# Performance work log

Hardware: AMD Instinct MI355X
Metric: run time of the kernel (lower is better)

## Reference

```python
import jax, jax.numpy as jnp
import numpy as np

B, T, M = 64, 32, 64
IN_DIM, GNN, H, L = 256, 256, 4, 3
TEMP, OUT, NH, NLT = 256, 512, 8, 2
DIST_THR = 0.3


def _ln(x, s, b, eps=1e-5):
    mu = jnp.mean(x, -1, keepdims=True)
    v = jnp.mean(jnp.square(x - mu), -1, keepdims=True)
    return (x - mu) * jax.lax.rsqrt(v + eps) * s + b


def setup_inputs() -> dict:
    key = jax.random.key(0)
    ks = iter(jax.random.split(key, 64))
    def nrm(shape, scale=0.05):
        return jax.random.normal(next(ks), shape, jnp.float32) * scale
    C = GNN // H
    return dict(
        drone_feats=jax.random.normal(next(ks), (B, T, M, IN_DIM), jnp.float32),
        boxes=jax.random.uniform(next(ks), (B, T, M, 5), jnp.float32),
        drone_mask=jnp.ones((B, T, M), jnp.float32),
        in_proj_W=nrm((GNN, IN_DIM)), in_proj_b=jnp.zeros((GNN,), jnp.float32),
        gat_lin_W=nrm((L, GNN, GNN)), gat_edge_W=nrm((L, 3, GNN)),
        gat_att_src=nrm((L, H, C)), gat_att_dst=nrm((L, H, C)), gat_att_edge=nrm((L, H, C)),
        gat_bias=jnp.zeros((L, GNN), jnp.float32),
        gat_ln_s=jnp.ones((L, GNN), jnp.float32), gat_ln_b=jnp.zeros((L, GNN), jnp.float32),
        temp_W=nrm((TEMP, GNN)), temp_b=jnp.zeros((TEMP,), jnp.float32),
        pos_emb=nrm((1, T, TEMP), 0.02),
        qkv_W=nrm((NLT, 3 * TEMP, TEMP)), qkv_b=jnp.zeros((NLT, 3 * TEMP), jnp.float32),
        attn_out_W=nrm((NLT, TEMP, TEMP)), attn_out_b=jnp.zeros((NLT, TEMP), jnp.float32),
        ln1_s=jnp.ones((NLT, TEMP), jnp.float32), ln1_b=jnp.zeros((NLT, TEMP), jnp.float32),
        ln2_s=jnp.ones((NLT, TEMP), jnp.float32), ln2_b=jnp.zeros((NLT, TEMP), jnp.float32),
        ff1_W=nrm((NLT, 2 * TEMP, TEMP)), ff1_b=jnp.zeros((NLT, 2 * TEMP), jnp.float32),
        ff2_W=nrm((NLT, TEMP, 2 * TEMP)), ff2_b=jnp.zeros((NLT, TEMP), jnp.float32),
        pool_W=nrm((1, TEMP)), pool_b=jnp.zeros((1,), jnp.float32),
        out_W=nrm((OUT, TEMP)), out_b=jnp.zeros((OUT,), jnp.float32),
        out_ln_s=jnp.ones((OUT,), jnp.float32), out_ln_b=jnp.zeros((OUT,), jnp.float32),
    )


def reference(drone_feats, boxes, drone_mask, in_proj_W, in_proj_b, gat_lin_W, gat_edge_W,
              gat_att_src, gat_att_dst, gat_att_edge, gat_bias, gat_ln_s, gat_ln_b,
              temp_W, temp_b, pos_emb, qkv_W, qkv_b, attn_out_W, attn_out_b,
              ln1_s, ln1_b, ln2_s, ln2_b, ff1_W, ff1_b, ff2_W, ff2_b,
              pool_W, pool_b, out_W, out_b, out_ln_s, out_ln_b):
    Bv, Tv, Mv, _ = drone_feats.shape
    Hh, Cc = gat_att_src.shape[1], gat_att_src.shape[2]
    valid = drone_mask > 0.5                                  # [B,T,M]

    # ---- batched radius-graph build (dense masked form over tiny M) ----
    pos = boxes[..., 1:3]                                     # [B,T,M,2]
    rel = pos[..., None, :, :] - pos[..., :, None, :]         # [B,T,s,d,2] = pos_d - pos_s
    sq = jnp.sum(jnp.square(rel), -1)
    dist = jnp.sqrt(jnp.maximum(sq, 1e-12))                   # [B,T,s,d]
    eye = jnp.eye(Mv, dtype=bool)
    pair_valid = valid[..., :, None] & valid[..., None, :]
    adj = pair_valid & (dist < DIST_THR) & (~eye)             # real directed edges (s->d)
    eattr = jnp.where(adj[..., None], jnp.concatenate([dist[..., None], rel], -1), 0.0)
    # GATConv(add_self_loops=True, fill_value='mean'): self-loop attr = mean incoming attr
    deg = jnp.maximum(jnp.sum(adj, axis=-2), 1).astype(eattr.dtype)   # incoming per dst
    loop_attr = jnp.sum(eattr, axis=-3) / deg[..., None]              # [B,T,M,3]
    eattr = jnp.where(eye[:, :, None], loop_attr[..., None, :, :], eattr)
    full_adj = adj | (eye & pair_valid)

    # ---- spatial GAT stack ----
    x = jnp.einsum('btmi,gi->btmg', drone_feats, in_proj_W) + in_proj_b
    x = x * valid[..., None]
    for l in range(gat_lin_W.shape[0]):
        h = jnp.einsum('btmg,gk->btmk', x, gat_lin_W[l]).reshape(Bv, Tv, Mv, Hh, Cc)
        a_src = jnp.einsum('btmhc,hc->btmh', h, gat_att_src[l])
        a_dst = jnp.einsum('btmhc,hc->btmh', h, gat_att_dst[l])
        w_e = jnp.einsum('ehc,hc->eh', gat_edge_W[l].reshape(3, Hh, Cc), gat_att_edge[l])
        a_edge = jnp.einsum('btsde,eh->btsdh', eattr, w_e)
        logits = a_src[..., :, None, :] + a_dst[..., None, :, :] + a_edge
        logits = jnp.where(logits >= 0, logits, 0.2 * logits)        # LeakyReLU(0.2)
        logits = jnp.where(full_adj[..., None], logits, jnp.float32(-1e9))
        alpha = jax.nn.softmax(logits, axis=-3)                      # softmax over src per dst
        msg = jnp.einsum('btsdh,btshc->btdhc', alpha, h).reshape(Bv, Tv, Mv, Hh * Cc) + gat_bias[l]
        x = jax.nn.relu(_ln(msg + x, gat_ln_s[l], gat_ln_b[l]))

    nvalid = jnp.maximum(jnp.sum(valid, -1), 1).astype(x.dtype)
    frame = jnp.sum(x * valid[..., None], axis=-2) / nvalid[..., None]   # [B,T,GNN]

    # ---- temporal transformer (norm_first, relu, 2 layers) ----
    y = jnp.einsum('btg,dg->btd', frame, temp_W) + temp_b
    y = y + pos_emb[:, :Tv, :]
    D = y.shape[-1]
    hd = D // NH
    for l in range(qkv_W.shape[0]):
        z = _ln(y, ln1_s[l], ln1_b[l])
        qkv = z @ qkv_W[l].T + qkv_b[l]
        q, k, v = jnp.split(qkv, 3, axis=-1)
        q = q.reshape(Bv, Tv, NH, hd).transpose(0, 2, 1, 3)
        k = k.reshape(Bv, Tv, NH, hd).transpose(0, 2, 1, 3)
        v = v.reshape(Bv, Tv, NH, hd).transpose(0, 2, 1, 3)
        att = jax.nn.softmax(jnp.einsum('bhqd,bhkd->bhqk', q, k) / jnp.sqrt(jnp.float32(hd)), -1)
        o = jnp.einsum('bhqk,bhkd->bhqd', att, v).transpose(0, 2, 1, 3).reshape(Bv, Tv, D)
        y = y + o @ attn_out_W[l].T + attn_out_b[l]
        z = _ln(y, ln2_s[l], ln2_b[l])
        y = y + jax.nn.relu(z @ ff1_W[l].T + ff1_b[l]) @ ff2_W[l].T + ff2_b[l]

    wts = jax.nn.softmax(y @ pool_W.T + pool_b, axis=1)   # [B,T,1]
    pooled = jnp.sum(y * wts, axis=1)                     # [B,D]
    out = pooled @ out_W.T + out_b
    return jax.nn.relu(_ln(out, out_ln_s, out_ln_b))
```

## Files before the change

kernel.cpp:

```cpp
#include <hip/hip_runtime.h>
#include <math.h>

#define BT 2048

typedef __attribute__((ext_vector_type(8))) short bf16x8;
typedef __attribute__((ext_vector_type(4))) float f32x4;
typedef __attribute__((ext_vector_type(4))) unsigned short u16x4;

__device__ inline unsigned short f2bf(float f) {
    union { float f; unsigned u; } v; v.f = f;
    unsigned r = (v.u >> 16) & 1u;
    return (unsigned short)((v.u + 0x7FFFu + r) >> 16);
}
__device__ inline float bf2f(unsigned short s) {
    union { unsigned u; float f; } v; v.u = ((unsigned)s) << 16;
    return v.f;
}

__device__ inline float dot4(const float4 a, const float4 b) {
    return fmaf(a.x, b.x, fmaf(a.y, b.y, fmaf(a.z, b.z, a.w * b.w)));
}

union F8 { float4 v2[2]; float f[8]; };

#define XP 264

__global__ __launch_bounds__(256) void k_prep(const float* __restrict__ inW,
                                              const float* __restrict__ gatW,
                                              unsigned short* __restrict__ dst) {
    int gid = blockIdx.x * 256 + threadIdx.x;
    int mat = gid >> 14;
    int r   = gid & 16383;
    int ks  = r >> 10;
    int nt  = (r >> 6) & 15;
    int lane = r & 63;
    int ln15 = lane & 15, q = lane >> 4;
    int n  = nt * 16 + ln15;
    int k0 = ks * 32 + q * 8;
    const float* src; bool tr;
    if (mat == 0) { src = inW; tr = true; }
    else          { src = gatW + (size_t)(mat - 1) * 65536; tr = false; }
    unsigned short* d = dst + ((size_t)mat * 16384 + r) * 16;
    if (ks < 8) {
        #pragma unroll
        for (int j = 0; j < 8; j++) {
            float v = tr ? src[n * 256 + k0 + j] : src[(size_t)(k0 + j) * 256 + n];
            unsigned short hi = f2bf(v);
            d[j]     = hi;
            d[8 + j] = f2bf(v - bf2f(hi));
        }
    } else {
        #pragma unroll
        for (int j = 0; j < 8; j++) { d[j] = 0; d[8 + j] = 0; }
    }
}

__global__ __launch_bounds__(1024, 4) void k_gnn(const float* __restrict__ feats,
                                                 const float* __restrict__ boxes,
                                                 const float* __restrict__ maskp,
                                                 const unsigned short* __restrict__ BswAll,
                                                 const float* __restrict__ inb,
                                                 const float* __restrict__ edgeW,
                                                 const float* __restrict__ attSg,
                                                 const float* __restrict__ attDg,
                                                 const float* __restrict__ attEg,
                                                 const float* __restrict__ gbias,
                                                 const float* __restrict__ glns,
                                                 const float* __restrict__ glnb,
                                                 float* __restrict__ framebuf) {
    int bt = blockIdx.x;
    size_t fbase = (size_t)bt * 64 * 256;

    __shared__ unsigned short xH[64 * XP];
    __shared__ unsigned short xL[64 * XP];
    __shared__ unsigned short hT[256 * 136];
    __shared__ float pxS[64], pyS[64], vmS[64];
    __shared__ float loopS[192];
    __shared__ float asrcS[16][64], adstS[16][64];
    __shared__ float wESall[36];
    __shared__ float sumsS[64][8];
    __shared__ float mrsS[64][2];
    __shared__ float nvS;

    int tid = threadIdx.x, lane = tid & 63, w = tid >> 6;
    int ln15 = lane & 15, q = lane >> 4;
    int nt = w;
    int eh = w >> 2;
    int dq = w & 3;

    if (tid < 64) {
        const float* bx = boxes + (size_t)(bt * 64 + tid) * 5;
        pxS[tid] = bx[1];
        pyS[tid] = bx[2];
        vmS[tid] = maskp[bt * 64 + tid];
    } else if (tid < 100) {
        int idx = tid - 64;
        int l = idx / 12, r2 = idx - l * 12;
        int e = r2 >> 2, h2 = r2 & 3;
        float sm = 0.f;
        const float* ew = edgeW + (size_t)l * 768 + e * 256 + h2 * 64;
        const float* ae = attEg + (size_t)l * 256 + h2 * 64;
        for (int c = 0; c < 64; c++) sm += ew[c] * ae[c];
        wESall[idx] = sm;
    }
    #pragma unroll
    for (int j = 0; j < 4; j++) {
        int g = j * 4096 + tid * 4;
        int row = g >> 8, col = g & 255;
        float4 v4 = *(const float4*)&feats[fbase + g];
        union { u16x4 v; unsigned short u[4]; } H4, L4;
        float vf[4] = {v4.x, v4.y, v4.z, v4.w};
        #pragma unroll
        for (int jj = 0; jj < 4; jj++) {
            H4.u[jj] = f2bf(vf[jj]);
            L4.u[jj] = f2bf(vf[jj] - bf2f(H4.u[jj]));
        }
        *(u16x4*)&xH[row * XP + col] = H4.v;
        *(u16x4*)&xL[row * XP + col] = L4.v;
    }
    __syncthreads();

    {
        int d = tid >> 4, part = tid & 15;
        float pxd = pxS[d], pyd = pyS[d];
        bool vd = vmS[d] > 0.5f;
        float deg = 0.f, s0 = 0.f, s1 = 0.f, s2 = 0.f;
        #pragma unroll
        for (int k = 0; k < 4; k++) {
            int s = part * 4 + k;
            float rx = pxd - pxS[s], ry = pyd - pyS[s];
            float dist = sqrtf(fmaxf(rx * rx + ry * ry, 1e-12f));
            bool adj = vd && (vmS[s] > 0.5f) && (dist < 0.3f) && (s != d);
            if (adj) { deg += 1.f; s0 += dist; s1 += rx; s2 += ry; }
        }
        #pragma unroll
        for (int off = 1; off < 16; off <<= 1) {
            deg += __shfl_xor(deg, off);
            s0  += __shfl_xor(s0, off);
            s1  += __shfl_xor(s1, off);
            s2  += __shfl_xor(s2, off);
        }
        if (part == 0) {
            float dg = fmaxf(deg, 1.f);
            loopS[d * 3 + 0] = s0 / dg;
            loopS[d * 3 + 1] = s1 / dg;
            loopS[d * 3 + 2] = s2 / dg;
        }
    }
    if (tid == 0) {
        float nv = 0.f;
        for (int m = 0; m < 64; m++) nv += vmS[m] > 0.5f ? 1.f : 0.f;
        nvS = fmaxf(nv, 1.f);
    }

    {
        f32x4 acc[4];
        #pragma unroll
        for (int mt = 0; mt < 4; mt++) acc[mt] = (f32x4){0.f, 0.f, 0.f, 0.f};
        for (int ks = 0; ks < 8; ks++) {
            const unsigned short* fb = &BswAll[((size_t)(ks * 16 + nt) * 64 + lane) * 16];
            bf16x8 bhi = *(const bf16x8*)&fb[0];
            bf16x8 blo = *(const bf16x8*)&fb[8];
            #pragma unroll
            for (int mt = 0; mt < 4; mt++) {
                int ao = (mt * 16 + ln15) * XP + ks * 32 + q * 8;
                bf16x8 ahi = *(const bf16x8*)&xH[ao];
                bf16x8 alo = *(const bf16x8*)&xL[ao];
                acc[mt] = __builtin_amdgcn_mfma_f32_16x16x32_bf16(ahi, bhi, acc[mt], 0, 0, 0);
                acc[mt] = __builtin_amdgcn_mfma_f32_16x16x32_bf16(alo, bhi, acc[mt], 0, 0, 0);
                acc[mt] = __builtin_amdgcn_mfma_f32_16x16x32_bf16(ahi, blo, acc[mt], 0, 0, 0);
            }
        }
        __syncthreads();
        int c = nt * 16 + ln15;
        float bv = inb[c];
        #pragma unroll
        for (int mt = 0; mt < 4; mt++) {
            #pragma unroll
            for (int r = 0; r < 4; r++) {
                int m = mt * 16 + q * 4 + r;
                float v = (acc[mt][r] + bv) * (vmS[m] > 0.5f ? 1.f : 0.f);
                unsigned short hi = f2bf(v);
                xH[m * XP + c] = hi;
                xL[m * XP + c] = f2bf(v - bf2f(hi));
            }
        }
    }
    __syncthreads();

    for (int l = 0; l < 3; l++) {
        const unsigned short* BswL = BswAll + (size_t)(1 + l) * 16384 * 16;
        const float* attSl = attSg + (size_t)l * 256;
        const float* attDl = attDg + (size_t)l * 256;
        const float* biasl = gbias + (size_t)l * 256;
        const float* lnsl  = glns + (size_t)l * 256;
        const float* lnbl  = glnb + (size_t)l * 256;
        const float* wES   = wESall + l * 12;

        f32x4 acc[4];
        #pragma unroll
        for (int mt = 0; mt < 4; mt++) acc[mt] = (f32x4){0.f, 0.f, 0.f, 0.f};
        for (int ks = 0; ks < 8; ks++) {
            const unsigned short* fb = &BswL[((size_t)(ks * 16 + nt) * 64 + lane) * 16];
            bf16x8 bhi = *(const bf16x8*)&fb[0];
            bf16x8 blo = *(const bf16x8*)&fb[8];
            #pragma unroll
            for (int mt = 0; mt < 4; mt++) {
                int ao = (mt * 16 + ln15) * XP + ks * 32 + q * 8;
                bf16x8 ahi = *(const bf16x8*)&xH[ao];
                bf16x8 alo = *(const bf16x8*)&xL[ao];
                acc[mt] = __builtin_amdgcn_mfma_f32_16x16x32_bf16(ahi, bhi, acc[mt], 0, 0, 0);
                acc[mt] = __builtin_amdgcn_mfma_f32_16x16x32_bf16(alo, bhi, acc[mt], 0, 0, 0);
                acc[mt] = __builtin_amdgcn_mfma_f32_16x16x32_bf16(ahi, blo, acc[mt], 0, 0, 0);
            }
        }

        {
            int c = nt * 16 + ln15;
            float aS = attSl[c], aD = attDl[c];
            float pS[4][4], pD[4][4];
            #pragma unroll
            for (int mt = 0; mt < 4; mt++) {
                union { u16x4 v; unsigned short u[4]; } HH, LL;
                #pragma unroll
                for (int r = 0; r < 4; r++) {
                    float v = acc[mt][r];
                    pS[mt][r] = v * aS;
                    pD[mt][r] = v * aD;
                    unsigned short hi = f2bf(v);
                    HH.u[r] = hi;
                    LL.u[r] = f2bf(v - bf2f(hi));
                }
                int s = mt * 16 + q * 4;
                *(u16x4*)&hT[c * 136 + s] = HH.v;
                *(u16x4*)&hT[c * 136 + 64 + s] = LL.v;
            }
            #pragma unroll
            for (int off = 1; off < 16; off <<= 1) {
                #pragma unroll
                for (int mt = 0; mt < 4; mt++)
                    #pragma unroll
                    for (int r = 0; r < 4; r++) {
                        pS[mt][r] += __shfl_xor(pS[mt][r], off);
                        pD[mt][r] += __shfl_xor(pD[mt][r], off);
                    }
            }
            if (ln15 == 0) {
                #pragma unroll
                for (int mt = 0; mt < 4; mt++)
                    #pragma unroll
                    for (int r = 0; r < 4; r++) {
                        int m = mt * 16 + q * 4 + r;
                        asrcS[w][m] = pS[mt][r];
                        adstS[w][m] = pD[mt][r];
                    }
            }
        }
        __syncthreads();

        f32x4 macc[4];
        #pragma unroll
        for (int ct = 0; ct < 4; ct++) macc[ct] = (f32x4){0.f, 0.f, 0.f, 0.f};
        {
            int d = dq * 16 + ln15;
            float pxd = pxS[d], pyd = pyS[d];
            bool vdv = vmS[d] > 0.5f;
            float adstv = adstS[4 * eh][d] + adstS[4 * eh + 1][d]
                        + adstS[4 * eh + 2][d] + adstS[4 * eh + 3][d];
            float lp0 = loopS[d * 3 + 0];
            float lp1 = loopS[d * 3 + 1];
            float lp2 = loopS[d * 3 + 2];
            float we0 = wES[eh], we1 = wES[4 + eh], we2 = wES[8 + eh];

            float lg[16];
            #pragma unroll
            for (int ks = 0; ks < 2; ks++) {
                int s0 = ks * 32 + q * 8;
                F8 PX, PY, VM, AU;
                PX.v2[0] = *(const float4*)&pxS[s0]; PX.v2[1] = *(const float4*)&pxS[s0 + 4];
                PY.v2[0] = *(const float4*)&pyS[s0]; PY.v2[1] = *(const float4*)&pyS[s0 + 4];
                VM.v2[0] = *(const float4*)&vmS[s0]; VM.v2[1] = *(const float4*)&vmS[s0 + 4];
                AU.v2[0] = *(const float4*)&asrcS[4 * eh][s0];
                AU.v2[1] = *(const float4*)&asrcS[4 * eh][s0 + 4];
                #pragma unroll
                for (int i = 1; i < 4; i++) {
                    float4 a0 = *(const float4*)&asrcS[4 * eh + i][s0];
                    float4 a1 = *(const float4*)&asrcS[4 * eh + i][s0 + 4];
                    AU.v2[0].x += a0.x; AU.v2[0].y += a0.y; AU.v2[0].z += a0.z; AU.v2[0].w += a0.w;
                    AU.v2[1].x += a1.x; AU.v2[1].y += a1.y; AU.v2[1].z += a1.z; AU.v2[1].w += a1.w;
                }
                #pragma unroll
                for (int j = 0; j < 8; j++) {
                    int s = s0 + j;
                    float vsf = VM.f[j];
                    float rx = pxd - PX.f[j], ry = pyd - PY.f[j];
                    float dist = sqrtf(fmaxf(rx * rx + ry * ry, 1e-12f));
                    bool self = (s == d);
                    bool adj = vdv && (vsf > 0.5f) && (dist < 0.3f) && !self;
                    float e0 = adj ? dist : (self ? lp0 : 0.f);
                    float e1 = adj ? rx   : (self ? lp1 : 0.f);
                    float e2 = adj ? ry   : (self ? lp2 : 0.f);
                    bool fa = adj || (self && vdv);
                    float lv = AU.f[j] + adstv + e0 * we0 + e1 * we1 + e2 * we2;
                    lv = lv >= 0.f ? lv : 0.2f * lv;
                    lg[ks * 8 + j] = fa ? lv : -1e9f;
                }
            }

            float mx = lg[0];
            #pragma unroll
            for (int j = 1; j < 16; j++) mx = fmaxf(mx, lg[j]);
            mx = fmaxf(mx, __shfl_xor(mx, 16));
            mx = fmaxf(mx, __shfl_xor(mx, 32));
            float sm = 0.f;
            #pragma unroll
            for (int j = 0; j < 16; j++) { lg[j] = __expf(lg[j] - mx); sm += lg[j]; }
            sm += __shfl_xor(sm, 16);
            sm += __shfl_xor(sm, 32);
            float inv = 1.f / sm;

            bf16x8 ah[2], al[2];
            #pragma unroll
            for (int ks2 = 0; ks2 < 2; ks2++) {
                union { bf16x8 v; unsigned short u[8]; } H, L;
                #pragma unroll
                for (int j = 0; j < 8; j++) {
                    float a = lg[ks2 * 8 + j] * inv;
                    unsigned short hi = f2bf(a);
                    H.u[j] = hi;
                    L.u[j] = f2bf(a - bf2f(hi));
                }
                ah[ks2] = H.v; al[ks2] = L.v;
            }

            #pragma unroll
            for (int ks2 = 0; ks2 < 2; ks2++) {
                #pragma unroll
                for (int ct = 0; ct < 4; ct++) {
                    const unsigned short* hb =
                        &hT[(size_t)(eh * 64 + ct * 16 + ln15) * 136 + ks2 * 32 + q * 8];
                    bf16x8 bhi = *(const bf16x8*)&hb[0];
                    bf16x8 blo = *(const bf16x8*)&hb[64];
                    macc[ct] = __builtin_amdgcn_mfma_f32_16x16x32_bf16(ah[ks2], bhi, macc[ct], 0, 0, 0);
                    macc[ct] = __builtin_amdgcn_mfma_f32_16x16x32_bf16(al[ks2], bhi, macc[ct], 0, 0, 0);
                    macc[ct] = __builtin_amdgcn_mfma_f32_16x16x32_bf16(ah[ks2], blo, macc[ct], 0, 0, 0);
                }
            }
        }

        {
            float bsv[4], scv[4], bbv[4];
            #pragma unroll
            for (int ct = 0; ct < 4; ct++) {
                int c = eh * 64 + ct * 16 + ln15;
                bsv[ct] = biasl[c];
                scv[ct] = lnsl[c];
                bbv[ct] = lnbl[c];
            }
            float xo[4][4];
            #pragma unroll
            for (int r = 0; r < 4; r++) {
                int d2 = dq * 16 + q * 4 + r;
                #pragma unroll
                for (int ct = 0; ct < 4; ct++) {
                    int o = d2 * XP + eh * 64 + ct * 16 + ln15;
                    xo[ct][r] = bf2f(xH[o]) + bf2f(xL[o]);
                }
            }
            float ps[4], ps2[4];
            #pragma unroll
            for (int r = 0; r < 4; r++) {
                float s = 0.f, s2 = 0.f;
                #pragma unroll
                for (int ct = 0; ct < 4; ct++) {
                    float v = macc[ct][r] + xo[ct][r] + bsv[ct];
                    s += v; s2 += v * v;
                }
                ps[r] = s; ps2[r] = s2;
            }
            #pragma unroll
            for (int off = 1; off < 16; off <<= 1) {
                #pragma unroll
                for (int i = 0; i < 4; i++) {
                    ps[i]  += __shfl_xor(ps[i], off);
                    ps2[i] += __shfl_xor(ps2[i], off);
                }
            }
            if (ln15 == 0) {
                #pragma unroll
                for (int r = 0; r < 4; r++) {
                    int d2 = dq * 16 + q * 4 + r;
                    sumsS[d2][eh * 2 + 0] = ps[r];
                    sumsS[d2][eh * 2 + 1] = ps2[r];
                }
            }
            __syncthreads();
            if (tid < 64) {
                float S  = sumsS[tid][0] + sumsS[tid][2] + sumsS[tid][4] + sumsS[tid][6];
                float S2 = sumsS[tid][1] + sumsS[tid][3] + sumsS[tid][5] + sumsS[tid][7];
                float mu = S * (1.f / 256.f);
                float var = S2 * (1.f / 256.f) - mu * mu;
                mrsS[tid][0] = mu;
                mrsS[tid][1] = rsqrtf(var + 1e-5f);
            }
            __syncthreads();
            #pragma unroll
            for (int r = 0; r < 4; r++) {
                int d2 = dq * 16 + q * 4 + r;
                float mu = mrsS[d2][0], rs = mrsS[d2][1];
                #pragma unroll
                for (int ct = 0; ct < 4; ct++) {
                    float v = (macc[ct][r] + xo[ct][r] + bsv[ct] - mu) * rs * scv[ct] + bbv[ct];
                    v = fmaxf(v, 0.f);
                    unsigned short hi = f2bf(v);
                    int o = d2 * XP + eh * 64 + ct * 16 + ln15;
                    xH[o] = hi;
                    xL[o] = f2bf(v - bf2f(hi));
                }
            }
        }
        __syncthreads();
    }

    if (tid < 256) {
        float s = 0.f;
        for (int m = 0; m < 64; m++) {
            float xv = bf2f(xH[m * XP + tid]) + bf2f(xL[m * XP + tid]);
            s += xv * (vmS[m] > 0.5f ? 1.f : 0.f);
        }
        framebuf[(size_t)bt * 256 + tid] = s / nvS;
    }
}

__global__ __launch_bounds__(256) void k_temp4(const float* __restrict__ framebuf,
                                               const float* __restrict__ tW,
                                               const float* __restrict__ tb,
                                               const float* __restrict__ pe,
                                               float* __restrict__ ybuf) {
    int b4 = blockIdx.x;
    int tid = threadIdx.x;
    __shared__ float frS[4][256];
    #pragma unroll
    for (int t = 0; t < 4; t++) frS[t][tid] = framebuf[(size_t)(b4 * 4 + t) * 256 + tid];
    __syncthreads();
    float acc[4];
    #pragma unroll
    for (int t = 0; t < 4; t++) acc[t] = tb[tid] + pe[((b4 * 4 + t) & 31) * 256 + tid];
    const float* wrow = tW + (size_t)tid * 256;
    for (int g = 0; g < 256; g += 4) {
        float4 wv = *(const float4*)&wrow[g];
        #pragma unroll
        for (int t = 0; t < 4; t++) acc[t] += dot4(*(const float4*)&frS[t][g], wv);
    }
    #pragma unroll
    for (int t = 0; t < 4; t++) ybuf[(size_t)(b4 * 4 + t) * 256 + tid] = acc[t];
}

__global__ __launch_bounds__(256) void k_ln_qkv4(const float* __restrict__ ybuf,
                                                 const float* __restrict__ ln_s,
                                                 const float* __restrict__ ln_b,
                                                 const float* __restrict__ qW,
                                                 const float* __restrict__ qb,
                                                 float* __restrict__ qkvbuf) {
    int b4 = blockIdx.x, tid = threadIdx.x;
    int lane = tid & 63, wv = tid >> 6;
    __shared__ float zS[4][256];
    {
        int bt = b4 * 4 + wv;
        float4 yv = *(const float4*)&ybuf[(size_t)bt * 256 + lane * 4];
        float s = yv.x + yv.y + yv.z + yv.w;
        float s2 = yv.x * yv.x + yv.y * yv.y + yv.z * yv.z + yv.w * yv.w;
        #pragma unroll
        for (int off = 1; off < 64; off <<= 1) { s += __shfl_xor(s, off); s2 += __shfl_xor(s2, off); }
        float mu = s * (1.f / 256.f);
        float var = s2 * (1.f / 256.f) - mu * mu;
        float rstd = rsqrtf(var + 1e-5f);
        float4 ls = *(const float4*)&ln_s[lane * 4];
        float4 lb = *(const float4*)&ln_b[lane * 4];
        float4 z;
        z.x = (yv.x - mu) * rstd * ls.x + lb.x;
        z.y = (yv.y - mu) * rstd * ls.y + lb.y;
        z.z = (yv.z - mu) * rstd * ls.z + lb.z;
        z.w = (yv.w - mu) * rstd * ls.w + lb.w;
        *(float4*)&zS[wv][lane * 4] = z;
    }
    __syncthreads();
    for (int r = 0; r < 3; r++) {
        int j = r * 256 + tid;
        float acc[4];
        float bv = qb[j];
        #pragma unroll
        for (int t = 0; t < 4; t++) acc[t] = bv;
        const float* wrow = qW + (size_t)j * 256;
        for (int i = 0; i < 256; i += 4) {
            float4 wv4 = *(const float4*)&wrow[i];
            #pragma unroll
            for (int t = 0; t < 4; t++) acc[t] += dot4(*(const float4*)&zS[t][i], wv4);
        }
        #pragma unroll
        for (int t = 0; t < 4; t++) qkvbuf[(size_t)(b4 * 4 + t) * 768 + j] = acc[t];
    }
}

__global__ __launch_bounds__(64) void k_attn(const float* __restrict__ qkvbuf,
                                             float* __restrict__ obuf) {
    int blk = blockIdx.x;
    int b = blk >> 3, h = blk & 7;
    int tid = threadIdx.x;
    __shared__ float Ks[32 * 32], Vs[32 * 32];
    for (int idx = tid; idx < 1024; idx += 64) {
        int tk = idx >> 5, c = idx & 31;
        size_t qbase = ((size_t)(b * 32 + tk)) * 768 + h * 32 + c;
        Ks[idx] = qkvbuf[qbase + 256];
        Vs[idx] = qkvbuf[qbase + 512];
    }
    __syncthreads();
    if (tid < 32) {
        int tq = tid;
        float qv[32];
        size_t qb0 = ((size_t)(b * 32 + tq)) * 768 + h * 32;
        #pragma unroll
        for (int c = 0; c < 32; c++) qv[c] = qkvbuf[qb0 + c];
        float scr[32];
        float mx = -1e30f;
        #pragma unroll
        for (int tk = 0; tk < 32; tk++) {
            float dd = 0.f;
            #pragma unroll
            for (int c = 0; c < 32; c++) dd = fmaf(qv[c], Ks[tk * 32 + c], dd);
            dd *= 0.17677669529663687f;
            scr[tk] = dd;
            mx = fmaxf(mx, dd);
        }
        float sm = 0.f;
        #pragma unroll
        for (int tk = 0; tk < 32; tk++) { scr[tk] = __expf(scr[tk] - mx); sm += scr[tk]; }
        float inv = 1.f / sm;
        float o[32];
        #pragma unroll
        for (int c = 0; c < 32; c++) o[c] = 0.f;
        #pragma unroll
        for (int tk = 0; tk < 32; tk++) {
            float a = scr[tk] * inv;
            #pragma unroll
            for (int c = 0; c < 32; c++) o[c] = fmaf(a, Vs[tk * 32 + c], o[c]);
        }
        size_t ob = ((size_t)(b * 32 + tq)) * 256 + h * 32;
        #pragma unroll
        for (int c = 0; c < 32; c++) obuf[ob + c] = o[c];
    }
}

__global__ __launch_bounds__(256) void k_attn_out4(const float* __restrict__ obuf,
                                                   const float* __restrict__ W,
                                                   const float* __restrict__ bvec,
                                                   float* __restrict__ ybuf) {
    int b4 = blockIdx.x, tid = threadIdx.x;
    int lane = tid & 63, wv = tid >> 6;
    __shared__ float oS[4][256];
    *(float4*)&oS[wv][lane * 4] = *(const float4*)&obuf[(size_t)(b4 * 4 + wv) * 256 + lane * 4];
    __syncthreads();
    float acc[4];
    float bv = bvec[tid];
    #pragma unroll
    for (int t = 0; t < 4; t++) acc[t] = bv;
    const float* wrow = W + (size_t)tid * 256;
    for (int i = 0; i < 256; i += 4) {
        float4 wv4 = *(const float4*)&wrow[i];
        #pragma unroll
        for (int t = 0; t < 4; t++) acc[t] += dot4(*(const float4*)&oS[t][i], wv4);
    }
    #pragma unroll
    for (int t = 0; t < 4; t++) ybuf[(size_t)(b4 * 4 + t) * 256 + tid] += acc[t];
}

__global__ __launch_bounds__(256) void k_ff4(float* __restrict__ ybuf,
                                             const float* __restrict__ ln_s,
                                             const float* __restrict__ ln_b,
                                             const float* __restrict__ W1,
                                             const float* __restrict__ b1,
                                             const float* __restrict__ W2,
                                             const float* __restrict__ b2) {
    int b4 = blockIdx.x, tid = threadIdx.x;
    int lane = tid & 63, wv = tid >> 6;
    __shared__ float zS[4][256];
    __shared__ float fS[4][512];
    {
        int bt = b4 * 4 + wv;
        float4 yv = *(const float4*)&ybuf[(size_t)bt * 256 + lane * 4];
        float s = yv.x + yv.y + yv.z + yv.w;
        float s2 = yv.x * yv.x + yv.y * yv.y + yv.z * yv.z + yv.w * yv.w;
        #pragma unroll
        for (int off = 1; off < 64; off <<= 1) { s += __shfl_xor(s, off); s2 += __shfl_xor(s2, off); }
        float mu = s * (1.f / 256.f);
        float var = s2 * (1.f / 256.f) - mu * mu;
        float rstd = rsqrtf(var + 1e-5f);
        float4 ls = *(const float4*)&ln_s[lane * 4];
        float4 lb = *(const float4*)&ln_b[lane * 4];
        float4 z;
        z.x = (yv.x - mu) * rstd * ls.x + lb.x;
        z.y = (yv.y - mu) * rstd * ls.y + lb.y;
        z.z = (yv.z - mu) * rstd * ls.z + lb.z;
        z.w = (yv.w - mu) * rstd * ls.w + lb.w;
        *(float4*)&zS[wv][lane * 4] = z;
    }
    __syncthreads();
    for (int r = 0; r < 2; r++) {
        int j = r * 256 + tid;
        float acc[4];
        float bv = b1[j];
        #pragma unroll
        for (int t = 0; t < 4; t++) acc[t] = bv;
        const float* wrow = W1 + (size_t)j * 256;
        for (int i = 0; i < 256; i += 4) {
            float4 wv4 = *(const float4*)&wrow[i];
            #pragma unroll
            for (int t = 0; t < 4; t++) acc[t] += dot4(*(const float4*)&zS[t][i], wv4);
        }
        #pragma unroll
        for (int t = 0; t < 4; t++) fS[t][j] = fmaxf(acc[t], 0.f);
    }
    __syncthreads();
    float acc[4];
    float bv = b2[tid];
    #pragma unroll
    for (int t = 0; t < 4; t++) acc[t] = bv;
    const float* wrow = W2 + (size_t)tid * 512;
    for (int jj = 0; jj < 512; jj += 4) {
        float4 wv4 = *(const float4*)&wrow[jj];
        #pragma unroll
        for (int t = 0; t < 4; t++) acc[t] += dot4(*(const float4*)&fS[t][jj], wv4);
    }
    #pragma unroll
    for (int t = 0; t < 4; t++) {
        size_t idx = (size_t)(b4 * 4 + t) * 256 + tid;
        ybuf[idx] = ybuf[idx] + acc[t];
    }
}

__global__ __launch_bounds__(256) void k_pool_out(const float* __restrict__ ybuf,
                                                  const float* __restrict__ pW,
                                                  const float* __restrict__ pb,
                                                  const float* __restrict__ oW,
                                                  const float* __restrict__ ob,
                                                  const float* __restrict__ lns,
                                                  const float* __restrict__ lnb,
                                                  float* __restrict__ dout) {
    int b = blockIdx.x, tid = threadIdx.x;
    __shared__ float redP[256];
    __shared__ float wS[32];
    __shared__ float pS[256];
    __shared__ float red[8];
    int tq = tid >> 3, part = tid & 7;
    float partial = 0.f;
    {
        const float* yrow = ybuf + ((size_t)(b * 32 + tq)) * 256 + part * 32;
        const float* pwp = pW + part * 32;
        #pragma unroll
        for (int j = 0; j < 32; j += 4) {
            float4 yv = *(const float4*)&yrow[j];
            float4 wv = *(const float4*)&pwp[j];
            partial += dot4(yv, wv);
        }
    }
    redP[tid] = partial;
    __syncthreads();
    if (tid < 32) {
        float s = pb[0];
        for (int p = 0; p < 8; p++) s += redP[tid * 8 + p];
        float mx = s;
        #pragma unroll
        for (int off = 16; off; off >>= 1) mx = fmaxf(mx, __shfl_xor(mx, off));
        float e = __expf(s - mx);
        float sm = e;
        #pragma unroll
        for (int off = 16; off; off >>= 1) sm += __shfl_xor(sm, off);
        wS[tid] = e / sm;
    }
    __syncthreads();
    float p = 0.f;
    for (int t = 0; t < 32; t++) p += ybuf[((size_t)(b * 32 + t)) * 256 + tid] * wS[t];
    pS[tid] = p;
    __syncthreads();
    float accs[2];
    for (int r = 0; r < 2; r++) {
        int j = r * 256 + tid;
        float acc = ob[j];
        const float* wrow = oW + (size_t)j * 256;
        for (int g = 0; g < 256; g += 4) {
            float4 pv = *(const float4*)&pS[g];
            float4 wv = *(const float4*)&wrow[g];
            acc += dot4(pv, wv);
        }
        accs[r] = acc;
    }
    float s = accs[0] + accs[1];
    float s2 = accs[0] * accs[0] + accs[1] * accs[1];
    #pragma unroll
    for (int off = 32; off; off >>= 1) {
        s += __shfl_xor(s, off);
        s2 += __shfl_xor(s2, off);
    }
    int wid = threadIdx.x >> 6;
    int lane = threadIdx.x & 63;
    if (lane == 0) { red[wid] = s; red[4 + wid] = s2; }
    __syncthreads();
    s = red[0] + red[1] + red[2] + red[3];
    s2 = red[4] + red[5] + red[6] + red[7];
    float mu = s * (1.f / 512.f);
    float var = s2 * (1.f / 512.f) - mu * mu;
    float rstd = rsqrtf(var + 1e-5f);
    dout[b * 512 + tid]       = fmaxf((accs[0] - mu) * rstd * lns[tid] + lnb[tid], 0.f);
    dout[b * 512 + tid + 256] = fmaxf((accs[1] - mu) * rstd * lns[tid + 256] + lnb[tid + 256], 0.f);
}

extern "C" void kernel_launch(void* const* d_in, const int* in_sizes, int n_in,
                              void* d_out, int out_size, void* d_ws, size_t ws_size,
                              hipStream_t stream) {
    const float* drone_feats = (const float*)d_in[0];
    const float* boxes       = (const float*)d_in[1];
    const float* drone_mask  = (const float*)d_in[2];
    const float* in_proj_W   = (const float*)d_in[3];
    const float* in_proj_b   = (const float*)d_in[4];
    const float* gat_lin_W   = (const float*)d_in[5];
    const float* gat_edge_W  = (const float*)d_in[6];
    const float* gat_att_src = (const float*)d_in[7];
    const float* gat_att_dst = (const float*)d_in[8];
    const float* gat_att_edge= (const float*)d_in[9];
    const float* gat_bias    = (const float*)d_in[10];
    const float* gat_ln_s    = (const float*)d_in[11];
    const float* gat_ln_b    = (const float*)d_in[12];
    const float* temp_W      = (const float*)d_in[13];
    const float* temp_b      = (const float*)d_in[14];
    const float* pos_emb     = (const float*)d_in[15];
    const float* qkv_W       = (const float*)d_in[16];
    const float* qkv_b       = (const float*)d_in[17];
    const float* attn_out_W  = (const float*)d_in[18];
    const float* attn_out_b  = (const float*)d_in[19];
    const float* ln1_s       = (const float*)d_in[20];
    const float* ln1_b       = (const float*)d_in[21];
    const float* ln2_s       = (const float*)d_in[22];
    const float* ln2_b       = (const float*)d_in[23];
    const float* ff1_W       = (const float*)d_in[24];
    const float* ff1_b       = (const float*)d_in[25];
    const float* ff2_W       = (const float*)d_in[26];
    const float* ff2_b       = (const float*)d_in[27];
    const float* pool_W      = (const float*)d_in[28];
    const float* pool_b      = (const float*)d_in[29];
    const float* out_W       = (const float*)d_in[30];
    const float* out_b       = (const float*)d_in[31];
    const float* out_ln_s    = (const float*)d_in[32];
    const float* out_ln_b    = (const float*)d_in[33];
    float* out = (float*)d_out;

    float* ws = (float*)d_ws;
    unsigned short* Bsw = (unsigned short*)ws;
    size_t off = (size_t)(4 * 16384 * 16) / 2;
    float* framebuf = ws + off; off += (size_t)BT * 256;
    float* ybuf   = ws + off; off += (size_t)BT * 256;
    float* qkvbuf = ws + off; off += (size_t)BT * 768;
    float* obuf   = ws + off; off += (size_t)BT * 256;

    k_prep<<<dim3(256), dim3(256), 0, stream>>>(in_proj_W, gat_lin_W, Bsw);
    k_gnn<<<dim3(BT), dim3(1024), 0, stream>>>(drone_feats, boxes, drone_mask, Bsw,
        in_proj_b, gat_edge_W, gat_att_src, gat_att_dst, gat_att_edge,
        gat_bias, gat_ln_s, gat_ln_b, framebuf);
    k_temp4<<<dim3(BT / 4), dim3(256), 0, stream>>>(framebuf, temp_W, temp_b, pos_emb, ybuf);
    for (int l = 0; l < 2; l++) {
        k_ln_qkv4<<<dim3(BT / 4), dim3(256), 0, stream>>>(ybuf, ln1_s + l * 256, ln1_b + l * 256,
            qkv_W + (size_t)l * 768 * 256, qkv_b + l * 768, qkvbuf);
        k_attn<<<dim3(512), dim3(64), 0, stream>>>(qkvbuf, obuf);
        k_attn_out4<<<dim3(BT / 4), dim3(256), 0, stream>>>(obuf,
            attn_out_W + (size_t)l * 65536, attn_out_b + l * 256, ybuf);
        k_ff4<<<dim3(BT / 4), dim3(256), 0, stream>>>(ybuf, ln2_s + l * 256, ln2_b + l * 256,
            ff1_W + (size_t)l * 131072, ff1_b + l * 512,
            ff2_W + (size_t)l * 131072, ff2_b + l * 256);
    }
    k_pool_out<<<dim3(64), dim3(256), 0, stream>>>(ybuf, pool_W, pool_b, out_W, out_b,
                                                   out_ln_s, out_ln_b, out);
}
```

Measured before the change: 1.133 ms.

## Fold attention projections into aux GEMM, alias LDS buffers, pack bf16 conversions

Precomputes W·att_src and W·att_dst per layer and head in a new prep kernel. Four extra waves then compute per-node attention logits with a small MFMA GEMM, which replaces the per-wave product and shuffle reduction. The hT buffer now shares LDS with xH/xL. To make that safe, the residual x plus bias is read into macc before a new barrier, and launch bounds are raised to allow more occupancy. Split-bf16 conversions now use the packed v_cvt_pk_bf16_f32 instruction, at the cost of extra MFMA work on four waves and one more barrier per layer.

New measurement: 1.142 ms. No clear change (+0.8%).

```diff
diff --git a/kernel.cpp b/kernel.cpp
--- a/kernel.cpp
+++ b/kernel.cpp
@@ -15,6 +15,14 @@
 __device__ inline float bf2f(unsigned short s) {
     union { unsigned u; float f; } v; v.u = ((unsigned)s) << 16;
     return v.f;
+}
+__device__ inline float ubf(unsigned u) {
+    union { unsigned u; float f; } v; v.u = u; return v.f;
+}
+__device__ inline unsigned cvt2(float a, float b) {
+    unsigned r;
+    asm("v_cvt_pk_bf16_f32 %0, %1, %2" : "=v"(r) : "v"(a), "v"(b));
+    return r;
 }
 
 __device__ inline float dot4(const float4 a, const float4 b) {
@@ -55,14 +63,39 @@
     }
 }
 
-__global__ __launch_bounds__(1024, 4) void k_gnn(const float* __restrict__ feats,
+__global__ __launch_bounds__(64) void k_prep_aux(const float* __restrict__ gatW,
+                                                 const float* __restrict__ attS,
+                                                 const float* __restrict__ attD,
+                                                 unsigned short* __restrict__ dst) {
+    int l  = blockIdx.x >> 3;
+    int ks = blockIdx.x & 7;
+    int lane = threadIdx.x;
+    int ln15 = lane & 15, q = lane >> 4;
+    int k0 = ks * 32 + q * 8;
+    const float* W = gatW + (size_t)l * 65536;
+    unsigned short* d = dst + ((size_t)(l * 8 + ks) * 64 + lane) * 16;
+    #pragma unroll
+    for (int j = 0; j < 8; j++) {
+        float v = 0.f;
+        if (ln15 < 8) {
+            int head = ln15 & 3;
+            const float* a = (ln15 < 4 ? attS : attD) + (size_t)l * 256 + head * 64;
+            const float* wr = W + (size_t)(k0 + j) * 256 + head * 64;
+            for (int c = 0; c < 64; c++) v = fmaf(wr[c], a[c], v);
+        }
+        unsigned short hi = f2bf(v);
+        d[j]     = hi;
+        d[8 + j] = f2bf(v - bf2f(hi));
+    }
+}
+
+__global__ __launch_bounds__(1024, 8) void k_gnn(const float* __restrict__ feats,
                                                  const float* __restrict__ boxes,
                                                  const float* __restrict__ maskp,
                                                  const unsigned short* __restrict__ BswAll,
+                                                 const unsigned short* __restrict__ auxB,
                                                  const float* __restrict__ inb,
                                                  const float* __restrict__ edgeW,
-                                                 const float* __restrict__ attSg,
-                                                 const float* __restrict__ attDg,
                                                  const float* __restrict__ attEg,
                                                  const float* __restrict__ gbias,
                                                  const float* __restrict__ glns,
@@ -71,16 +104,17 @@
     int bt = blockIdx.x;
     size_t fbase = (size_t)bt * 64 * 256;
 
-    __shared__ unsigned short xH[64 * XP];
-    __shared__ unsigned short xL[64 * XP];
-    __shared__ unsigned short hT[256 * 136];
+    __shared__ __align__(16) unsigned short U[256 * 136];
     __shared__ float pxS[64], pyS[64], vmS[64];
     __shared__ float loopS[192];
-    __shared__ float asrcS[16][64], adstS[16][64];
+    __shared__ float asrcS[4][64], adstS[4][64];
     __shared__ float wESall[36];
     __shared__ float sumsS[64][8];
     __shared__ float mrsS[64][2];
     __shared__ float nvS;
+
+    unsigned short* xH = U;
+    unsigned short* xL = U + 64 * XP;
 
     int tid = threadIdx.x, lane = tid & 63, w = tid >> 6;
     int ln15 = lane & 15, q = lane >> 4;
@@ -108,15 +142,16 @@
         int g = j * 4096 + tid * 4;
         int row = g >> 8, col = g & 255;
         float4 v4 = *(const float4*)&feats[fbase + g];
-        union { u16x4 v; unsigned short u[4]; } H4, L4;
-        float vf[4] = {v4.x, v4.y, v4.z, v4.w};
-        #pragma unroll
-        for (int jj = 0; jj < 4; jj++) {
-            H4.u[jj] = f2bf(vf[jj]);
-            L4.u[jj] = f2bf(vf[jj] - bf2f(H4.u[jj]));
-        }
-        *(u16x4*)&xH[row * XP + col] = H4.v;
-        *(u16x4*)&xL[row * XP + col] = L4.v;
+        unsigned p0 = cvt2(v4.x, v4.y);
+        unsigned p1 = cvt2(v4.z, v4.w);
+        float h0 = ubf(p0 << 16), h1 = ubf(p0 & 0xFFFF0000u);
+        float h2 = ubf(p1 << 16), h3 = ubf(p1 & 0xFFFF0000u);
+        unsigned l0 = cvt2(v4.x - h0, v4.y - h1);
+        unsigned l1 = cvt2(v4.z - h2, v4.w - h3);
+        *(unsigned*)&xH[row * XP + col]     = p0;
+        *(unsigned*)&xH[row * XP + col + 2] = p1;
+        *(unsigned*)&xL[row * XP + col]     = l0;
+        *(unsigned*)&xL[row * XP + col + 2] = l1;
     }
     __syncthreads();
 
@@ -190,8 +225,6 @@
 
     for (int l = 0; l < 3; l++) {
         const unsigned short* BswL = BswAll + (size_t)(1 + l) * 16384 * 16;
-        const float* attSl = attSg + (size_t)l * 256;
-        const float* attDl = attDg + (size_t)l * 256;
         const float* biasl = gbias + (size_t)l * 256;
         const float* lnsl  = glns + (size_t)l * 256;
         const float* lnbl  = glnb + (size_t)l * 256;
@@ -215,58 +248,68 @@
             }
         }
 
+        if (w >= 12) {
+            int mm = w - 12;
+            f32x4 aax = (f32x4){0.f, 0.f, 0.f, 0.f};
+            const unsigned short* AuxL = auxB + (size_t)l * 8 * 64 * 16;
+            for (int ks = 0; ks < 8; ks++) {
+                const unsigned short* fb = &AuxL[((size_t)ks * 64 + lane) * 16];
+                bf16x8 bhi = *(const bf16x8*)&fb[0];
+                bf16x8 blo = *(const bf16x8*)&fb[8];
+                int ao = (mm * 16 + ln15) * XP + ks * 32 + q * 8;
+                bf16x8 ahi = *(const bf16x8*)&xH[ao];
+                bf16x8 alo = *(const bf16x8*)&xL[ao];
+                aax = __builtin_amdgcn_mfma_f32_16x16x32_bf16(ahi, bhi, aax, 0, 0, 0);
+                aax = __builtin_amdgcn_mfma_f32_16x16x32_bf16(alo, bhi, aax, 0, 0, 0);
+                aax = __builtin_amdgcn_mfma_f32_16x16x32_bf16(ahi, blo, aax, 0, 0, 0);
+            }
+            if (ln15 < 4) {
+                #pragma unroll
+                for (int r = 0; r < 4; r++) asrcS[ln15][mm * 16 + q * 4 + r] = aax[r];
+            } else if (ln15 < 8) {
+                #pragma unroll
+                for (int r = 0; r < 4; r++) adstS[ln15 - 4][mm * 16 + q * 4 + r] = aax[r];
+            }
+        }
+
+        f32x4 macc[4];
+        #pragma unroll
+        for (int ct = 0; ct < 4; ct++) {
+            int c = eh * 64 + ct * 16 + ln15;
+            float bv = biasl[c];
+            #pragma unroll
+            for (int r = 0; r < 4; r++) {
+                int d2 = dq * 16 + q * 4 + r;
+                int o = d2 * XP + c;
+                macc[ct][r] = bf2f(xH[o]) + bf2f(xL[o]) + bv;
+            }
+        }
+        __syncthreads();
+
         {
             int c = nt * 16 + ln15;
-            float aS = attSl[c], aD = attDl[c];
-            float pS[4][4], pD[4][4];
             #pragma unroll
             for (int mt = 0; mt < 4; mt++) {
-                union { u16x4 v; unsigned short u[4]; } HH, LL;
-                #pragma unroll
-                for (int r = 0; r < 4; r++) {
-                    float v = acc[mt][r];
-                    pS[mt][r] = v * aS;
-                    pD[mt][r] = v * aD;
-                    unsigned short hi = f2bf(v);
-                    HH.u[r] = hi;
-                    LL.u[r] = f2bf(v - bf2f(hi));
-                }
+                unsigned p0 = cvt2(acc[mt][0], acc[mt][1]);
+                unsigned p1 = cvt2(acc[mt][2], acc[mt][3]);
+                float h0 = ubf(p0 << 16), h1 = ubf(p0 & 0xFFFF0000u);
+                float h2 = ubf(p1 << 16), h3 = ubf(p1 & 0xFFFF0000u);
+                unsigned l0 = cvt2(acc[mt][0] - h0, acc[mt][1] - h1);
+                unsigned l1 = cvt2(acc[mt][2] - h2, acc[mt][3] - h3);
                 int s = mt * 16 + q * 4;
-                *(u16x4*)&hT[c * 136 + s] = HH.v;
-                *(u16x4*)&hT[c * 136 + 64 + s] = LL.v;
-            }
-            #pragma unroll
-            for (int off = 1; off < 16; off <<= 1) {
-                #pragma unroll
-                for (int mt = 0; mt < 4; mt++)
-                    #pragma unroll
-                    for (int r = 0; r < 4; r++) {
-                        pS[mt][r] += __shfl_xor(pS[mt][r], off);
-                        pD[mt][r] += __shfl_xor(pD[mt][r], off);
-                    }
-            }
-            if (ln15 == 0) {
-                #pragma unroll
-                for (int mt = 0; mt < 4; mt++)
-                    #pragma unroll
-                    for (int r = 0; r < 4; r++) {
-                        int m = mt * 16 + q * 4 + r;
-                        asrcS[w][m] = pS[mt][r];
-                        adstS[w][m] = pD[mt][r];
-                    }
+                *(unsigned*)&U[c * 136 + s]          = p0;
+                *(unsigned*)&U[c * 136 + s + 2]      = p1;
+                *(unsigned*)&U[c * 136 + 64 + s]     = l0;
+                *(unsigned*)&U[c * 136 + 64 + s + 2] = l1;
             }
         }
         __syncthreads();
 
-        f32x4 macc[4];
-        #pragma unroll
-        for (int ct = 0; ct < 4; ct++) macc[ct] = (f32x4){0.f, 0.f, 0.f, 0.f};
         {
             int d = dq * 16 + ln15;
             float pxd = pxS[d], pyd = pyS[d];
             bool vdv = vmS[d] > 0.5f;
-            float adstv = adstS[4 * eh][d] + adstS[4 * eh + 1][d]
-                        + adstS[4 * eh + 2][d] + adstS[4 * eh + 3][d];
+            float adstv = adstS[eh][d];
             float lp0 = loopS[d * 3 + 0];
             float lp1 = loopS[d * 3 + 1];
             float lp2 = loopS[d * 3 + 2];
@@ -276,19 +319,12 @@
             #pragma unroll
             for (int ks = 0; ks < 2; ks++) {
                 int s0 = ks * 32 + q * 8;
-                F8 PX, PY, VM, AU;
+                F8 PX, PY, VM, AS;
                 PX.v2[0] = *(const float4*)&pxS[s0]; PX.v2[1] = *(const float4*)&pxS[s0 + 4];
                 PY.v2[0] = *(const float4*)&pyS[s0]; PY.v2[1] = *(const float4*)&pyS[s0 + 4];
                 VM.v2[0] = *(const float4*)&vmS[s0]; VM.v2[1] = *(const float4*)&vmS[s0 + 4];
-                AU.v2[0] = *(const float4*)&asrcS[4 * eh][s0];
-                AU.v2[1] = *(const float4*)&asrcS[4 * eh][s0 + 4];
-                #pragma unroll
-                for (int i = 1; i < 4; i++) {
-                    float4 a0 = *(const float4*)&asrcS[4 * eh + i][s0];
-                    float4 a1 = *(const float4*)&asrcS[4 * eh + i][s0 + 4];
-                    AU.v2[0].x += a0.x; AU.v2[0].y += a0.y; AU.v2[0].z += a0.z; AU.v2[0].w += a0.w;
-                    AU.v2[1].x += a1.x; AU.v2[1].y += a1.y; AU.v2[1].z += a1.z; AU.v2[1].w += a1.w;
-                }
+                AS.v2[0] = *(const float4*)&asrcS[eh][s0];
+                AS.v2[1] = *(const float4*)&asrcS[eh][s0 + 4];
                 #pragma unroll
                 for (int j = 0; j < 8; j++) {
                     int s = s0 + j;
@@ -301,7 +337,7 @@
                     float e1 = adj ? rx   : (self ? lp1 : 0.f);
                     float e2 = adj ? ry   : (self ? lp2 : 0.f);
                     bool fa = adj || (self && vdv);
-                    float lv = AU.f[j] + adstv + e0 * we0 + e1 * we1 + e2 * we2;
+                    float lv = AS.f[j] + adstv + e0 * we0 + e1 * we1 + e2 * we2;
                     lv = lv >= 0.f ? lv : 0.2f * lv;
                     lg[ks * 8 + j] = fa ? lv : -1e9f;
                 }
@@ -322,13 +358,15 @@
             bf16x8 ah[2], al[2];
             #pragma unroll
             for (int ks2 = 0; ks2 < 2; ks2++) {
-                union { bf16x8 v; unsigned short u[8]; } H, L;
+                union { bf16x8 v; unsigned u[4]; } H, L;
                 #pragma unroll
-                for (int j = 0; j < 8; j++) {
-                    float a = lg[ks2 * 8 + j] * inv;
-                    unsigned short hi = f2bf(a);
-                    H.u[j] = hi;
-                    L.u[j] = f2bf(a - bf2f(hi));
+                for (int jj = 0; jj < 4; jj++) {
+                    float a0 = lg[ks2 * 8 + jj * 2] * inv;
+                    float a1 = lg[ks2 * 8 + jj * 2 + 1] * inv;
+                    unsigned p = cvt2(a0, a1);
+                    H.u[jj] = p;
+                    float f0 = ubf(p << 16), f1 = ubf(p & 0xFFFF0000u);
+                    L.u[jj] = cvt2(a0 - f0, a1 - f1);
                 }
                 ah[ks2] = H.v; al[ks2] = L.v;
             }
@@ -338,7 +376,7 @@
                 #pragma unroll
                 for (int ct = 0; ct < 4; ct++) {
                     const unsigned short* hb =
-                        &hT[(size_t)(eh * 64 + ct * 16 + ln15) * 136 + ks2 * 32 + q * 8];
+                        &U[(size_t)(eh * 64 + ct * 16 + ln15) * 136 + ks2 * 32 + q * 8];
                     bf16x8 bhi = *(const bf16x8*)&hb[0];
                     bf16x8 blo = *(const bf16x8*)&hb[64];
                     macc[ct] = __builtin_amdgcn_mfma_f32_16x16x32_bf16(ah[ks2], bhi, macc[ct], 0, 0, 0);
@@ -349,23 +387,12 @@
         }
 
         {
-            float bsv[4], scv[4], bbv[4];
+            float scv[4], bbv[4];
             #pragma unroll
             for (int ct = 0; ct < 4; ct++) {
                 int c = eh * 64 + ct * 16 + ln15;
-                bsv[ct] = biasl[c];
                 scv[ct] = lnsl[c];
                 bbv[ct] = lnbl[c];
-            }
-            float xo[4][4];
-            #pragma unroll
-            for (int r = 0; r < 4; r++) {
-                int d2 = dq * 16 + q * 4 + r;
-                #pragma unroll
-                for (int ct = 0; ct < 4; ct++) {
-                    int o = d2 * XP + eh * 64 + ct * 16 + ln15;
-                    xo[ct][r] = bf2f(xH[o]) + bf2f(xL[o]);
-                }
             }
             float ps[4], ps2[4];
             #pragma unroll
@@ -373,7 +400,7 @@
                 float s = 0.f, s2 = 0.f;
                 #pragma unroll
                 for (int ct = 0; ct < 4; ct++) {
-                    float v = macc[ct][r] + xo[ct][r] + bsv[ct];
+                    float v = macc[ct][r];
                     s += v; s2 += v * v;
                 }
                 ps[r] = s; ps2[r] = s2;
@@ -410,7 +437,7 @@
                 float mu = mrsS[d2][0], rs = mrsS[d2][1];
                 #pragma unroll
                 for (int ct = 0; ct < 4; ct++) {
-                    float v = (macc[ct][r] + xo[ct][r] + bsv[ct] - mu) * rs * scv[ct] + bbv[ct];
+                    float v = (macc[ct][r] - mu) * rs * scv[ct] + bbv[ct];
                     v = fmaxf(v, 0.f);
                     unsigned short hi = f2bf(v);
                     int o = d2 * XP + eh * 64 + ct * 16 + ln15;
@@ -754,16 +781,18 @@
     float* out = (float*)d_out;
 
     float* ws = (float*)d_ws;
-    unsigned short* Bsw = (unsigned short*)ws;
-    size_t off = (size_t)(4 * 16384 * 16) / 2;
+    unsigned short* Bsw    = (unsigned short*)ws;
+    unsigned short* BswAux = Bsw + (size_t)4 * 16384 * 16;
+    size_t off = ((size_t)4 * 16384 * 16 + 3 * 8 * 64 * 16 + 1) / 2;
     float* framebuf = ws + off; off += (size_t)BT * 256;
     float* ybuf   = ws + off; off += (size_t)BT * 256;
     float* qkvbuf = ws + off; off += (size_t)BT * 768;
     float* obuf   = ws + off; off += (size_t)BT * 256;
 
     k_prep<<<dim3(256), dim3(256), 0, stream>>>(in_proj_W, gat_lin_W, Bsw);
-    k_gnn<<<dim3(BT), dim3(1024), 0, stream>>>(drone_feats, boxes, drone_mask, Bsw,
-        in_proj_b, gat_edge_W, gat_att_src, gat_att_dst, gat_att_edge,
+    k_prep_aux<<<dim3(24), dim3(64), 0, stream>>>(gat_lin_W, gat_att_src, gat_att_dst, BswAux);
+    k_gnn<<<dim3(BT), dim3(1024), 0, stream>>>(drone_feats, boxes, drone_mask, Bsw, BswAux,
+        in_proj_b, gat_edge_W, gat_att_edge,
         gat_bias, gat_ln_s, gat_ln_b, framebuf);
     k_temp4<<<dim3(BT / 4), dim3(256), 0, stream>>>(framebuf, temp_W, temp_b, pos_emb, ybuf);
     for (int l = 0; l < 2; l++) {
```
